# Performance work log

Hardware: AMD Instinct MI355X
Metric: run time of the kernel (lower is better)

## Reference

```python
import jax, jax.numpy as jnp
import numpy as np

NUM_HEADS = 16


def setup_inputs() -> dict:
    key = jax.random.key(0)
    k1, k2, k3, k4, k5 = jax.random.split(key, 5)
    B, N, E = 16, 8, 2048
    H = NUM_HEADS
    D = E // H
    KV = 4096
    return {
        "x": jax.random.normal(k1, (B, N, E), dtype=jnp.float32),
        "past_k": jax.random.normal(k2, (B, H, KV, D), dtype=jnp.float32),
        "past_v": jax.random.normal(k3, (B, H, KV, D), dtype=jnp.float32),
        "W_qkv": jax.random.normal(k4, (3 * E, E), dtype=jnp.float32) * (E ** -0.5),
        "W_out": jax.random.normal(k5, (E, E), dtype=jnp.float32) * (E ** -0.5),
    }


def reference(x, past_k, past_v, W_qkv, W_out):
    B, N, E = x.shape
    H = NUM_HEADS
    D = E // H
    # fused QKV projection: [B, N, 3E]
    qkv = jnp.einsum("bne,fe->bnf", x, W_qkv)
    q, k_new, v_new = jnp.split(qkv, 3, axis=-1)
    # '... n (h d) -> ... h n d'
    to_heads = lambda t: t.reshape(B, N, H, D).swapaxes(1, 2)
    q, k_new, v_new = to_heads(q), to_heads(k_new), to_heads(v_new)
    # KV cache append along seq dim
    k = jnp.concatenate([past_k, k_new], axis=-2)  # [B, H, KV+N, D]
    v = jnp.concatenate([past_v, v_new], axis=-2)
    # SDPA (eval mode -> is_causal=False)
    scale = D ** -0.5
    scores = jnp.einsum("bhqd,bhkd->bhqk", q, k) * scale
    attn = jax.nn.softmax(scores, axis=-1)
    out = jnp.einsum("bhqk,bhkd->bhqd", attn, v)  # [B, H, N, D]
    # '... h n d -> ... n (h d)'
    out = out.swapaxes(1, 2).reshape(B, N, E)
    out = jnp.einsum("bne,fe->bnf", out, W_out)
    return (out, k, v)
```

## Files before the change

kernel.cpp:

```cpp
#include <hip/hip_runtime.h>
#include <cstddef>
#include <cstdint>

#define B_ 16
#define H_ 16
#define NQ 8
#define D_ 128
#define E_ 2048
#define F3 6144
#define KVP 4096
#define KVT 4104
#define SCALE 0.08838834764831843f
#define NCHUNK 8
#define CHUNK 512
#define SUBR 32
#define NSUB 16
#define PARTSZ 1040

template <int BM, int BN>
__global__ __launch_bounds__(256) void gemm_xwt(const float* __restrict__ X,
                                                const float* __restrict__ W,
                                                float* __restrict__ C,
                                                int K, int Fdim) {
  constexpr int BK = 32;
  constexpr int RM = BM / 16;
  constexpr int RN = BN / 16;
  __shared__ float xs[BK][BM + 4];
  __shared__ float wss[BK][BN + 4];
  const int t = threadIdx.x;
  const int tm = t >> 4, tn = t & 15;
  const int m0 = blockIdx.y * BM, f0 = blockIdx.x * BN;
  float acc[RM][RN];
#pragma unroll
  for (int i = 0; i < RM; ++i)
#pragma unroll
    for (int j = 0; j < RN; ++j) acc[i][j] = 0.f;

  for (int kk = 0; kk < K; kk += BK) {
#pragma unroll
    for (int i = 0; i < (BM * BK) / 1024; ++i) {
      int j = t + i * 256;
      int r = j >> 3;
      int c = (j & 7) << 2;
      float4 v = *reinterpret_cast<const float4*>(&X[(size_t)(m0 + r) * K + kk + c]);
      xs[c + 0][r] = v.x; xs[c + 1][r] = v.y; xs[c + 2][r] = v.z; xs[c + 3][r] = v.w;
    }
#pragma unroll
    for (int i = 0; i < (BN * BK) / 1024; ++i) {
      int j = t + i * 256;
      int r = j >> 3;
      int c = (j & 7) << 2;
      float4 v = *reinterpret_cast<const float4*>(&W[(size_t)(f0 + r) * K + kk + c]);
      wss[c + 0][r] = v.x; wss[c + 1][r] = v.y; wss[c + 2][r] = v.z; wss[c + 3][r] = v.w;
    }
    __syncthreads();
#pragma unroll
    for (int k = 0; k < BK; ++k) {
      float xv[RM], wv[RN];
      if constexpr (RM == 4) {
        *reinterpret_cast<float4*>(xv) = *reinterpret_cast<const float4*>(&xs[k][tm * 4]);
      } else {
        *reinterpret_cast<float2*>(xv) = *reinterpret_cast<const float2*>(&xs[k][tm * 2]);
      }
      if constexpr (RN == 4) {
        *reinterpret_cast<float4*>(wv) = *reinterpret_cast<const float4*>(&wss[k][tn * 4]);
      } else {
        *reinterpret_cast<float2*>(wv) = *reinterpret_cast<const float2*>(&wss[k][tn * 2]);
      }
#pragma unroll
      for (int i = 0; i < RM; ++i)
#pragma unroll
        for (int j = 0; j < RN; ++j) acc[i][j] += xv[i] * wv[j];
    }
    __syncthreads();
  }
#pragma unroll
  for (int i = 0; i < RM; ++i) {
    float* cp = &C[(size_t)(m0 + tm * RM + i) * Fdim + f0 + tn * RN];
    if constexpr (RN == 4) {
      *reinterpret_cast<float4*>(cp) = make_float4(acc[i][0], acc[i][1], acc[i][2], acc[i][3]);
    } else {
      *reinterpret_cast<float2*>(cp) = make_float2(acc[i][0], acc[i][1]);
    }
  }
}

__global__ __launch_bounds__(256) void attn_partial(
    const float* __restrict__ past_k, const float* __restrict__ past_v,
    const float* __restrict__ qkv, float* __restrict__ out_k,
    float* __restrict__ out_v, float* __restrict__ part) {
  const int t = threadIdx.x;
  const int c = blockIdx.x, h = blockIdx.y, b = blockIdx.z;
  const int bh = b * H_ + h;
  const int g = t & 31, rg = t >> 5;

  __shared__ float red[4096];
  __shared__ float f_lds[NQ];
  __shared__ float m_lds[2][NQ], l_lds[2][NQ];
  float* s_lds = red;
  float* p_lds = red + 288;

  float4 qreg[NQ];
#pragma unroll
  for (int qi = 0; qi < NQ; ++qi)
    qreg[qi] = *reinterpret_cast<const float4*>(
        &qkv[(size_t)(b * NQ + qi) * F3 + h * D_ + g * 4]);

  if (t < NQ) { m_lds[0][t] = -1e30f; l_lds[0][t] = 0.f; }

  const float* gk = past_k + ((size_t)bh * KVP + (size_t)c * CHUNK) * D_;
  const float* gv = past_v + ((size_t)bh * KVP + (size_t)c * CHUNK) * D_;
  float* ok = out_k + ((size_t)bh * KVT + (size_t)c * CHUNK) * D_;
  float* ov = out_v + ((size_t)bh * KVT + (size_t)c * CHUNK) * D_;

  float4 acc[NQ];
#pragma unroll
  for (int qi = 0; qi < NQ; ++qi) acc[qi] = make_float4(0.f, 0.f, 0.f, 0.f);

  const int b0 = g & 1, b1 = (g >> 1) & 1, b2 = (g >> 2) & 1;
  const int qsel = 4 * b0 + 2 * b1 + b2;

  __syncthreads();

  for (int sub = 0; sub < NSUB; ++sub) {
    const int cur = sub & 1, nxt = cur ^ 1;
    const size_t off = (size_t)sub * SUBR * D_;

    float4 kf[4], vf[4];
#pragma unroll
    for (int i = 0; i < 4; ++i) {
      const size_t ga = off + (size_t)(rg + 8 * i) * D_ + g * 4;
      kf[i] = *reinterpret_cast<const float4*>(&gk[ga]);
      vf[i] = *reinterpret_cast<const float4*>(&gv[ga]);
    }
#pragma unroll
    for (int i = 0; i < 4; ++i) {
      const int r = rg + 8 * i;
      const size_t ga = off + (size_t)r * D_ + g * 4;
      *reinterpret_cast<float4*>(&ok[ga]) = kf[i];
      *reinterpret_cast<float4*>(&ov[ga]) = vf[i];
      float sp[NQ];
#pragma unroll
      for (int qi = 0; qi < NQ; ++qi)
        sp[qi] = kf[i].x * qreg[qi].x + kf[i].y * qreg[qi].y +
                 kf[i].z * qreg[qi].z + kf[i].w * qreg[qi].w;
      float v1[4];
#pragma unroll
      for (int j = 0; j < 4; ++j) {
        float x = b0 ? sp[j] : sp[j + 4];
        v1[j] = (b0 ? sp[j + 4] : sp[j]) + __shfl_xor(x, 1);
      }
      float v2[2];
#pragma unroll
      for (int j = 0; j < 2; ++j) {
        float x = b1 ? v1[j] : v1[j + 2];
        v2[j] = (b1 ? v1[j + 2] : v1[j]) + __shfl_xor(x, 2);
      }
      float v3;
      {
        float x = b2 ? v2[0] : v2[1];
        v3 = (b2 ? v2[1] : v2[0]) + __shfl_xor(x, 4);
      }
      v3 += __shfl_xor(v3, 8);
      v3 += __shfl_xor(v3, 16);
      if (g < 8) s_lds[r * 9 + qsel] = v3;
    }
    __syncthreads();

    {
      const int srow = t & 31, sqi = t >> 5;
      float s = s_lds[srow * 9 + sqi] * SCALE;
      float cmax = s;
#pragma unroll
      for (int o = 16; o > 0; o >>= 1) cmax = fmaxf(cmax, __shfl_xor(cmax, o));
      float mo = m_lds[cur][sqi];
      float mn = fmaxf(mo, cmax);
      float p = __expf(s - mn);
      float psum = p;
#pragma unroll
      for (int o = 16; o > 0; o >>= 1) psum += __shfl_xor(psum, o);
      p_lds[srow * 8 + sqi] = p;
      if (srow == 0) {
        float f = __expf(mo - mn);
        f_lds[sqi] = f;
        m_lds[nxt][sqi] = mn;
        l_lds[nxt][sqi] = l_lds[cur][sqi] * f + psum;
      }
    }
    __syncthreads();

    {
      float4 f0 = *reinterpret_cast<const float4*>(&f_lds[0]);
      float4 f1 = *reinterpret_cast<const float4*>(&f_lds[4]);
      acc[0].x *= f0.x; acc[0].y *= f0.x; acc[0].z *= f0.x; acc[0].w *= f0.x;
      acc[1].x *= f0.y; acc[1].y *= f0.y; acc[1].z *= f0.y; acc[1].w *= f0.y;
      acc[2].x *= f0.z; acc[2].y *= f0.z; acc[2].z *= f0.z; acc[2].w *= f0.z;
      acc[3].x *= f0.w; acc[3].y *= f0.w; acc[3].z *= f0.w; acc[3].w *= f0.w;
      acc[4].x *= f1.x; acc[4].y *= f1.x; acc[4].z *= f1.x; acc[4].w *= f1.x;
      acc[5].x *= f1.y; acc[5].y *= f1.y; acc[5].z *= f1.y; acc[5].w *= f1.y;
      acc[6].x *= f1.z; acc[6].y *= f1.z; acc[6].z *= f1.z; acc[6].w *= f1.z;
      acc[7].x *= f1.w; acc[7].y *= f1.w; acc[7].z *= f1.w; acc[7].w *= f1.w;
#pragma unroll
      for (int i = 0; i < 4; ++i) {
        const int r = rg + 8 * i;
        float4 pa = *reinterpret_cast<const float4*>(&p_lds[r * 8]);
        float4 pc = *reinterpret_cast<const float4*>(&p_lds[r * 8 + 4]);
        acc[0].x += pa.x * vf[i].x; acc[0].y += pa.x * vf[i].y; acc[0].z += pa.x * vf[i].z; acc[0].w += pa.x * vf[i].w;
        acc[1].x += pa.y * vf[i].x; acc[1].y += pa.y * vf[i].y; acc[1].z += pa.y * vf[i].z; acc[1].w += pa.y * vf[i].w;
        acc[2].x += pa.z * vf[i].x; acc[2].y += pa.z * vf[i].y; acc[2].z += pa.z * vf[i].z; acc[2].w += pa.z * vf[i].w;
        acc[3].x += pa.w * vf[i].x; acc[3].y += pa.w * vf[i].y; acc[3].z += pa.w * vf[i].z; acc[3].w += pa.w * vf[i].w;
        acc[4].x += pc.x * vf[i].x; acc[4].y += pc.x * vf[i].y; acc[4].z += pc.x * vf[i].z; acc[4].w += pc.x * vf[i].w;
        acc[5].x += pc.y * vf[i].x; acc[5].y += pc.y * vf[i].y; acc[5].z += pc.y * vf[i].z; acc[5].w += pc.y * vf[i].w;
        acc[6].x += pc.z * vf[i].x; acc[6].y += pc.z * vf[i].y; acc[6].z += pc.z * vf[i].z; acc[6].w += pc.z * vf[i].w;
        acc[7].x += pc.w * vf[i].x; acc[7].y += pc.w * vf[i].y; acc[7].z += pc.w * vf[i].z; acc[7].w += pc.w * vf[i].w;
      }
    }
  }

  __syncthreads();

#pragma unroll
  for (int half = 4; half >= 1; half >>= 1) {
    if (rg >= half && rg < 2 * half) {
#pragma unroll
      for (int qi = 0; qi < NQ; ++qi)
        *reinterpret_cast<float4*>(&red[(rg - half) * 1024 + qi * 128 + g * 4]) = acc[qi];
    }
    __syncthreads();
    if (rg < half) {
#pragma unroll
      for (int qi = 0; qi < NQ; ++qi) {
        float4 o = *reinterpret_cast<const float4*>(&red[rg * 1024 + qi * 128 + g * 4]);
        acc[qi].x += o.x; acc[qi].y += o.y; acc[qi].z += o.z; acc[qi].w += o.w;
      }
    }
    __syncthreads();
  }

  float* pb = part + ((size_t)bh * NCHUNK + c) * PARTSZ;
  if (t < NQ) { pb[t] = m_lds[0][t]; pb[8 + t] = l_lds[0][t]; }
  if (rg == 0) {
#pragma unroll
    for (int qi = 0; qi < NQ; ++qi)
      *reinterpret_cast<float4*>(&pb[16 + qi * 128 + g * 4]) = acc[qi];
  }
}

__global__ __launch_bounds__(256) void attn_combine(
    const float* __restrict__ qkv, const float* __restrict__ part,
    float* __restrict__ out_k, float* __restrict__ out_v,
    float* __restrict__ attn) {
  const int t = threadIdx.x;
  const int h = blockIdx.x, b = blockIdx.y;
  const int bh = b * H_ + h;
  __shared__ float q_lds[NQ * 132];
  __shared__ float kn_lds[NQ * 132];
  __shared__ float vn_lds[NQ * 132];
  __shared__ float p9[NQ * 12];
  __shared__ float m9_lds[NQ], s9_lds[NQ];
  {
    int n = t >> 5, g = t & 31;
    const float* src = &qkv[(size_t)(b * NQ + n) * F3 + h * D_ + g * 4];
    float4 qv = *reinterpret_cast<const float4*>(src);
    float4 kv = *reinterpret_cast<const float4*>(src + E_);
    float4 vv = *reinterpret_cast<const float4*>(src + 2 * E_);
    *reinterpret_cast<float4*>(&q_lds[n * 132 + g * 4]) = qv;
    *reinterpret_cast<float4*>(&kn_lds[n * 132 + g * 4]) = kv;
    *reinterpret_cast<float4*>(&vn_lds[n * 132 + g * 4]) = vv;
    *reinterpret_cast<float4*>(&out_k[((size_t)bh * KVT + KVP + n) * D_ + g * 4]) = kv;
    *reinterpret_cast<float4*>(&out_v[((size_t)bh * KVT + KVP + n) * D_ + g * 4]) = vv;
  }
  __syncthreads();
  if (t < 64) {
    int nq = t >> 3, nk = t & 7;
    float s = 0.f;
#pragma unroll
    for (int g = 0; g < 32; ++g) {
      float4 qv = *reinterpret_cast<const float4*>(&q_lds[nq * 132 + g * 4]);
      float4 kv = *reinterpret_cast<const float4*>(&kn_lds[nk * 132 + g * 4]);
      s += qv.x * kv.x + qv.y * kv.y + qv.z * kv.z + qv.w * kv.w;
    }
    s *= SCALE;
    float mx = s;
#pragma unroll
    for (int o = 4; o > 0; o >>= 1) mx = fmaxf(mx, __shfl_xor(mx, o));
    float p = __expf(s - mx);
    float sm = p;
#pragma unroll
    for (int o = 4; o > 0; o >>= 1) sm += __shfl_xor(sm, o);
    p9[nk * 12 + nq] = p;
    if (nk == 0) { m9_lds[nq] = mx; s9_lds[nq] = sm; }
  }
  __syncthreads();
  const int qg = t >> 7, dcol = t & 127;
  const float* pb = part + (size_t)bh * NCHUNK * PARTSZ;
#pragma unroll
  for (int jq = 0; jq < 4; ++jq) {
    int qi = qg * 4 + jq;
    float M = m9_lds[qi];
#pragma unroll
    for (int c = 0; c < NCHUNK; ++c) M = fmaxf(M, pb[(size_t)c * PARTSZ + qi]);
    float num = 0.f, den = 0.f;
#pragma unroll
    for (int c = 0; c < NCHUNK; ++c) {
      const float* pc = pb + (size_t)c * PARTSZ;
      float wgt = __expf(pc[qi] - M);
      den += wgt * pc[8 + qi];
      num += wgt * pc[16 + (size_t)qi * D_ + dcol];
    }
    float acc9 = 0.f;
#pragma unroll
    for (int r = 0; r < NQ; ++r) acc9 += p9[r * 12 + qi] * vn_lds[r * 132 + dcol];
    float w9 = __expf(m9_lds[qi] - M);
    num += w9 * acc9;
    den += w9 * s9_lds[qi];
    attn[((size_t)(b * NQ + qi)) * E_ + h * D_ + dcol] = num / den;
  }
}

extern "C" void kernel_launch(void* const* d_in, const int* in_sizes, int n_in,
                              void* d_out, int out_size, void* d_ws, size_t ws_size,
                              hipStream_t stream) {
  const float* x      = (const float*)d_in[0];
  const float* past_k = (const float*)d_in[1];
  const float* past_v = (const float*)d_in[2];
  const float* W_qkv  = (const float*)d_in[3];
  const float* W_out  = (const float*)d_in[4];

  float* out   = (float*)d_out;
  float* out_k = out + (size_t)B_ * NQ * E_;
  float* out_v = out_k + (size_t)B_ * H_ * KVT * D_;

  float* ws   = (float*)d_ws;
  float* qkv  = ws;
  float* part = qkv + (size_t)B_ * NQ * F3;
  float* attn = part + (size_t)B_ * H_ * NCHUNK * PARTSZ;

  gemm_xwt<64, 32><<<dim3(F3 / 32, 128 / 64), 256, 0, stream>>>(x, W_qkv, qkv, E_, F3);
  attn_partial<<<dim3(NCHUNK, H_, B_), 256, 0, stream>>>(past_k, past_v, qkv, out_k, out_v, part);
  attn_combine<<<dim3(H_, B_), 256, 0, stream>>>(qkv, part, out_k, out_v, attn);
  gemm_xwt<32, 32><<<dim3(E_ / 32, 128 / 32), 256, 0, stream>>>(attn, W_out, out, E_, E_);
}
```

Before: 609.1 us.

## Split-K GEMMs, prefetch KV tiles, and non-temporal KV cache stores

The QKV and output projections now use 64x64 tiles with an optional split-K of 2 when the workspace is large enough. Partial sums are combined inside the attention kernels, or by a small add kernel for the output projection. The attention kernel software-pipelines the K/V loads by prefetching the next sub-tile into a second register set after the barrier. It also writes the copied KV cache with non-temporal stores to avoid polluting the cache. This costs more registers, an extra launch and extra workspace traffic.

```diff
diff --git a/kernel.cpp b/kernel.cpp
--- a/kernel.cpp
+++ b/kernel.cpp
@@ -17,7 +17,15 @@
 #define NSUB 16
 #define PARTSZ 1040
 
-template <int BM, int BN>
+typedef float f32x4_t __attribute__((ext_vector_type(4)));
+
+__device__ __forceinline__ void nt_store4(float* p, float4 v) {
+  f32x4_t w;
+  w.x = v.x; w.y = v.y; w.z = v.z; w.w = v.w;
+  __builtin_nontemporal_store(w, reinterpret_cast<f32x4_t*>(p));
+}
+
+template <int BM, int BN, int SPLITK>
 __global__ __launch_bounds__(256) void gemm_xwt(const float* __restrict__ X,
                                                 const float* __restrict__ W,
                                                 float* __restrict__ C,
@@ -30,13 +38,16 @@
   const int t = threadIdx.x;
   const int tm = t >> 4, tn = t & 15;
   const int m0 = blockIdx.y * BM, f0 = blockIdx.x * BN;
+  const int kbeg = (SPLITK > 1) ? blockIdx.z * (K / SPLITK) : 0;
+  const int kend = (SPLITK > 1) ? kbeg + K / SPLITK : K;
+  if (SPLITK > 1) C += (size_t)blockIdx.z * 128 * Fdim;
   float acc[RM][RN];
 #pragma unroll
   for (int i = 0; i < RM; ++i)
 #pragma unroll
     for (int j = 0; j < RN; ++j) acc[i][j] = 0.f;
 
-  for (int kk = 0; kk < K; kk += BK) {
+  for (int kk = kbeg; kk < kend; kk += BK) {
 #pragma unroll
     for (int i = 0; i < (BM * BK) / 1024; ++i) {
       int j = t + i * 256;
@@ -85,10 +96,21 @@
   }
 }
 
+__global__ __launch_bounds__(256) void add2(const float* __restrict__ a,
+                                            const float* __restrict__ b,
+                                            float* __restrict__ o) {
+  int i = blockIdx.x * 256 + threadIdx.x;
+  float4 va = reinterpret_cast<const float4*>(a)[i];
+  float4 vb = reinterpret_cast<const float4*>(b)[i];
+  reinterpret_cast<float4*>(o)[i] =
+      make_float4(va.x + vb.x, va.y + vb.y, va.z + vb.z, va.w + vb.w);
+}
+
 __global__ __launch_bounds__(256) void attn_partial(
     const float* __restrict__ past_k, const float* __restrict__ past_v,
-    const float* __restrict__ qkv, float* __restrict__ out_k,
-    float* __restrict__ out_v, float* __restrict__ part) {
+    const float* __restrict__ qkv_a, const float* __restrict__ qkv_b,
+    float* __restrict__ out_k, float* __restrict__ out_v,
+    float* __restrict__ part) {
   const int t = threadIdx.x;
   const int c = blockIdx.x, h = blockIdx.y, b = blockIdx.z;
   const int bh = b * H_ + h;
@@ -102,9 +124,15 @@
 
   float4 qreg[NQ];
 #pragma unroll
-  for (int qi = 0; qi < NQ; ++qi)
-    qreg[qi] = *reinterpret_cast<const float4*>(
-        &qkv[(size_t)(b * NQ + qi) * F3 + h * D_ + g * 4]);
+  for (int qi = 0; qi < NQ; ++qi) {
+    const size_t qoff = (size_t)(b * NQ + qi) * F3 + h * D_ + g * 4;
+    float4 q0 = *reinterpret_cast<const float4*>(&qkv_a[qoff]);
+    if (qkv_b) {
+      float4 q1 = *reinterpret_cast<const float4*>(&qkv_b[qoff]);
+      q0.x += q1.x; q0.y += q1.y; q0.z += q1.z; q0.w += q1.w;
+    }
+    qreg[qi] = q0;
+  }
 
   if (t < NQ) { m_lds[0][t] = -1e30f; l_lds[0][t] = 0.f; }
 
@@ -120,25 +148,26 @@
   const int b0 = g & 1, b1 = (g >> 1) & 1, b2 = (g >> 2) & 1;
   const int qsel = 4 * b0 + 2 * b1 + b2;
 
-  __syncthreads();
-
-  for (int sub = 0; sub < NSUB; ++sub) {
-    const int cur = sub & 1, nxt = cur ^ 1;
+  auto loadf = [&](float4 (&kf)[4], float4 (&vf)[4], int sub) {
     const size_t off = (size_t)sub * SUBR * D_;
-
-    float4 kf[4], vf[4];
 #pragma unroll
     for (int i = 0; i < 4; ++i) {
       const size_t ga = off + (size_t)(rg + 8 * i) * D_ + g * 4;
       kf[i] = *reinterpret_cast<const float4*>(&gk[ga]);
       vf[i] = *reinterpret_cast<const float4*>(&gv[ga]);
     }
+  };
+
+  auto bodyf = [&](float4 (&kf)[4], float4 (&vf)[4], float4 (&kfN)[4],
+                   float4 (&vfN)[4], int sub, bool pf) {
+    const int cur = sub & 1, nxt = cur ^ 1;
+    const size_t off = (size_t)sub * SUBR * D_;
 #pragma unroll
     for (int i = 0; i < 4; ++i) {
       const int r = rg + 8 * i;
       const size_t ga = off + (size_t)r * D_ + g * 4;
-      *reinterpret_cast<float4*>(&ok[ga]) = kf[i];
-      *reinterpret_cast<float4*>(&ov[ga]) = vf[i];
+      nt_store4(&ok[ga], kf[i]);
+      nt_store4(&ov[ga], vf[i]);
       float sp[NQ];
 #pragma unroll
       for (int qi = 0; qi < NQ; ++qi)
@@ -188,6 +217,8 @@
       }
     }
     __syncthreads();
+
+    if (pf) loadf(kfN, vfN, sub + 1);
 
     {
       float4 f0 = *reinterpret_cast<const float4*>(&f_lds[0]);
@@ -215,6 +246,15 @@
         acc[7].x += pc.w * vf[i].x; acc[7].y += pc.w * vf[i].y; acc[7].z += pc.w * vf[i].z; acc[7].w += pc.w * vf[i].w;
       }
     }
+  };
+
+  __syncthreads();
+
+  float4 kfA[4], vfA[4], kfB[4], vfB[4];
+  loadf(kfA, vfA, 0);
+  for (int sub = 0; sub < NSUB; sub += 2) {
+    bodyf(kfA, vfA, kfB, vfB, sub, true);
+    bodyf(kfB, vfB, kfA, vfA, sub + 1, sub + 2 < NSUB);
   }
 
   __syncthreads();
@@ -247,9 +287,9 @@
 }
 
 __global__ __launch_bounds__(256) void attn_combine(
-    const float* __restrict__ qkv, const float* __restrict__ part,
-    float* __restrict__ out_k, float* __restrict__ out_v,
-    float* __restrict__ attn) {
+    const float* __restrict__ qkv_a, const float* __restrict__ qkv_b,
+    const float* __restrict__ part, float* __restrict__ out_k,
+    float* __restrict__ out_v, float* __restrict__ attn) {
   const int t = threadIdx.x;
   const int h = blockIdx.x, b = blockIdx.y;
   const int bh = b * H_ + h;
@@ -260,10 +300,18 @@
   __shared__ float m9_lds[NQ], s9_lds[NQ];
   {
     int n = t >> 5, g = t & 31;
-    const float* src = &qkv[(size_t)(b * NQ + n) * F3 + h * D_ + g * 4];
-    float4 qv = *reinterpret_cast<const float4*>(src);
-    float4 kv = *reinterpret_cast<const float4*>(src + E_);
-    float4 vv = *reinterpret_cast<const float4*>(src + 2 * E_);
+    const size_t soff = (size_t)(b * NQ + n) * F3 + h * D_ + g * 4;
+    float4 qv = *reinterpret_cast<const float4*>(&qkv_a[soff]);
+    float4 kv = *reinterpret_cast<const float4*>(&qkv_a[soff + E_]);
+    float4 vv = *reinterpret_cast<const float4*>(&qkv_a[soff + 2 * E_]);
+    if (qkv_b) {
+      float4 q1 = *reinterpret_cast<const float4*>(&qkv_b[soff]);
+      float4 k1 = *reinterpret_cast<const float4*>(&qkv_b[soff + E_]);
+      float4 v1 = *reinterpret_cast<const float4*>(&qkv_b[soff + 2 * E_]);
+      qv.x += q1.x; qv.y += q1.y; qv.z += q1.z; qv.w += q1.w;
+      kv.x += k1.x; kv.y += k1.y; kv.z += k1.z; kv.w += k1.w;
+      vv.x += v1.x; vv.y += v1.y; vv.z += v1.z; vv.w += v1.w;
+    }
     *reinterpret_cast<float4*>(&q_lds[n * 132 + g * 4]) = qv;
     *reinterpret_cast<float4*>(&kn_lds[n * 132 + g * 4]) = kv;
     *reinterpret_cast<float4*>(&vn_lds[n * 132 + g * 4]) = vv;
@@ -331,13 +379,32 @@
   float* out_k = out + (size_t)B_ * NQ * E_;
   float* out_v = out_k + (size_t)B_ * H_ * KVT * D_;
 
-  float* ws   = (float*)d_ws;
-  float* qkv  = ws;
-  float* part = qkv + (size_t)B_ * NQ * F3;
-  float* attn = part + (size_t)B_ * H_ * NCHUNK * PARTSZ;
-
-  gemm_xwt<64, 32><<<dim3(F3 / 32, 128 / 64), 256, 0, stream>>>(x, W_qkv, qkv, E_, F3);
-  attn_partial<<<dim3(NCHUNK, H_, B_), 256, 0, stream>>>(past_k, past_v, qkv, out_k, out_v, part);
-  attn_combine<<<dim3(H_, B_), 256, 0, stream>>>(qkv, part, out_k, out_v, attn);
-  gemm_xwt<32, 32><<<dim3(E_ / 32, 128 / 32), 256, 0, stream>>>(attn, W_out, out, E_, E_);
-}
+  const size_t QKV_N  = (size_t)B_ * NQ * F3;
+  const size_t PART_N = (size_t)B_ * H_ * NCHUNK * PARTSZ;
+  const size_t ATTN_N = (size_t)B_ * NQ * E_;
+  const size_t need2  = (2 * QKV_N + PART_N + 3 * ATTN_N) * sizeof(float);
+
+  float* ws = (float*)d_ws;
+  const bool split2 = ws_size >= need2;
+
+  float* pq0  = ws;
+  float* pq1  = split2 ? ws + QKV_N : nullptr;
+  float* part = ws + (split2 ? 2 : 1) * QKV_N;
+  float* attn = part + PART_N;
+  float* po0  = attn + ATTN_N;
+
+  if (split2) {
+    gemm_xwt<64, 64, 2><<<dim3(F3 / 64, 2, 2), 256, 0, stream>>>(x, W_qkv, pq0, E_, F3);
+  } else {
+    gemm_xwt<64, 64, 1><<<dim3(F3 / 64, 2), 256, 0, stream>>>(x, W_qkv, pq0, E_, F3);
+  }
+  attn_partial<<<dim3(NCHUNK, H_, B_), 256, 0, stream>>>(past_k, past_v, pq0, pq1,
+                                                         out_k, out_v, part);
+  attn_combine<<<dim3(H_, B_), 256, 0, stream>>>(pq0, pq1, part, out_k, out_v, attn);
+  if (split2) {
+    gemm_xwt<64, 64, 2><<<dim3(E_ / 64, 2, 2), 256, 0, stream>>>(attn, W_out, po0, E_, E_);
+    add2<<<dim3(ATTN_N / 1024), 256, 0, stream>>>(po0, po0 + ATTN_N, out);
+  } else {
+    gemm_xwt<64, 64, 1><<<dim3(E_ / 64, 2), 256, 0, stream>>>(attn, W_out, out, E_, E_);
+  }
+}
```

After: 568.0 us. -6.8%, faster.
